# Kernel optimization log

Hardware: AMD Instinct MI355X
Metric: run time of the kernel (lower is better)

## Reference

```python
import jax, jax.numpy as jnp
import numpy as np

B, N, D, E = 8, 512, 256, 16384  # batch, num_nodes, hidden_dim, num_edges


def setup_inputs() -> dict:
    key = jax.random.key(0)
    kf, ke, k1, k2, k3, k4 = jax.random.split(key, 6)
    features = jax.random.normal(kf, (B, N, D), dtype=jnp.float32)
    edge_index = jax.random.randint(ke, (2, E), 0, N, dtype=jnp.int64)
    # weight_net: Linear(2D -> D), ReLU, Linear(D -> 1), Sigmoid
    s1 = 1.0 / np.sqrt(2 * D)
    s2 = 1.0 / np.sqrt(D)
    W1 = jax.random.uniform(k1, (2 * D, D), jnp.float32, -s1, s1)
    b1 = jax.random.uniform(k2, (D,), jnp.float32, -s1, s1)
    W2 = jax.random.uniform(k3, (D, 1), jnp.float32, -s2, s2)
    b2 = jax.random.uniform(k4, (1,), jnp.float32, -s2, s2)
    return {"features": features, "W1": W1, "b1": b1, "W2": W2, "b2": b2,
            "edge_index": edge_index}


def reference(features, W1, b1, W2, b2, edge_index):
    src, dst = edge_index[0], edge_index[1]            # [E], [E]
    fi = features[:, src]                              # [B, E, D]
    fj = features[:, dst]                              # [B, E, D]
    pair = jnp.concatenate([fi, fj], axis=-1)          # [B, E, 2D]
    h = jax.nn.relu(jnp.einsum('bef,fh->beh', pair, W1) + b1)   # [B, E, D]
    s = jax.nn.sigmoid(jnp.einsum('beh,ho->beo', h, W2) + b2)[..., 0]  # [B, E]
    bsz, n = features.shape[0], features.shape[1]
    weights = jnp.zeros((bsz, n, n), features.dtype).at[:, src, dst].set(s)
    return weights
```

## Files before the change

kernel.cpp:

```cpp
#include <hip/hip_runtime.h>
#include <hip/hip_bf16.h>
#include <cstdint>

#define B_ 8
#define N_ 512
#define D_ 256
#define E_ 16384
#define H_ 256

#define SA_STRIDE 56
#define SB_STRIDE 56
#define NSB 8
#define SUBCAP 32

using bf16x8 = __attribute__((ext_vector_type(8))) short;
using f32x4  = __attribute__((ext_vector_type(4))) float;

__device__ inline unsigned short f2bf(float f) {
    union { float f; unsigned u; } v; v.f = f;
    unsigned u = v.u;
    return (unsigned short)((u + 0x7fffu + ((u >> 16) & 1u)) >> 16);
}

__global__ __launch_bounds__(256)
void prep_k(const float* __restrict__ W1, const int* __restrict__ eidx,
            unsigned short* __restrict__ W1T,
            int* __restrict__ gCnt, int* __restrict__ gBucket) {
    const int tb = blockIdx.x, t = threadIdx.x;

    if (tb >= 32) {
        __shared__ int hist[512];
        const int sb = tb - 32;
        for (int i = t; i < 512; i += 256) hist[i] = 0;
        __syncthreads();
#pragma unroll
        for (int k = 0; k < 8; k++) {
            int e = sb * 2048 + k * 256 + t;
            int s = eidx[e];
            int d = eidx[E_ + e];
            int slot = atomicAdd(&hist[s], 1);
            gBucket[(s * NSB + sb) * SUBCAP + slot] = d;
        }
        __syncthreads();
        for (int s = t; s < 512; s += 256)
            gCnt[s * NSB + sb] = hist[s];
        return;
    }

    __shared__ float tile[64][65];
    const int h   = tb >> 4;
    const int rem = tb & 15;
    const int tk  = (rem >> 2) * 64;
    const int tn  = (rem & 3) * 64;
    const float* Wh = W1 + (size_t)h * 256 * 256;
    const int c = t & 63, r0 = t >> 6;
#pragma unroll
    for (int i = 0; i < 16; i++) {
        int r = r0 + i * 4;
        tile[r][c] = Wh[(size_t)(tk + r) * 256 + tn + c];
    }
    __syncthreads();
#pragma unroll
    for (int i = 0; i < 16; i++) {
        int rn = r0 + i * 4;
        W1T[(size_t)(h * 256 + tn + rn) * 256 + tk + c] = f2bf(tile[c][rn]);
    }
}

__global__ __launch_bounds__(256)
void node_gemm(const float* __restrict__ feat,
               const unsigned short* __restrict__ W1T,
               const float* __restrict__ b1,
               unsigned short* __restrict__ P,
               float4* __restrict__ out4) {
    __shared__ unsigned short sA[64 * SA_STRIDE];
    __shared__ unsigned short sB[256 * SB_STRIDE];

    const int t  = threadIdx.x;
    const int bm = blockIdx.x >> 1;
    const int bn = blockIdx.x & 1;
    const int m0 = bm * 64;

    {
        float4 z = make_float4(0.f, 0.f, 0.f, 0.f);
        float4* oz = out4 + (size_t)blockIdx.x * 4096 + t;
#pragma unroll
        for (int i = 0; i < 16; i++) oz[i * 256] = z;
    }

    const int arow = t >> 2;
    const int akg  = (t & 3) * 8;
    const float* pA = feat + (size_t)(m0 + arow) * 256;
    const unsigned short* pB = W1T + (size_t)(bn * 256 + t) * 256;

    const int wave = t >> 6, lane = t & 63, l15 = lane & 15, quad = lane >> 4;

    f32x4 acc[4][4];
#pragma unroll
    for (int rm = 0; rm < 4; rm++)
#pragma unroll
        for (int cn = 0; cn < 4; cn++)
            acc[rm][cn] = (f32x4){0.f, 0.f, 0.f, 0.f};

    for (int k0 = 0; k0 < 256; k0 += 32) {
        __syncthreads();
        {
            float4 lo = *(const float4*)(pA + k0 + akg);
            float4 hi = *(const float4*)(pA + k0 + akg + 4);
            union { bf16x8 v; unsigned short s[8]; } u;
            u.s[0] = f2bf(lo.x); u.s[1] = f2bf(lo.y); u.s[2] = f2bf(lo.z); u.s[3] = f2bf(lo.w);
            u.s[4] = f2bf(hi.x); u.s[5] = f2bf(hi.y); u.s[6] = f2bf(hi.z); u.s[7] = f2bf(hi.w);
            *(bf16x8*)(sA + arow * SA_STRIDE + akg) = u.v;
        }
        {
            const unsigned short* p = pB + k0;
            uint4 q0 = *(const uint4*)(p);
            uint4 q1 = *(const uint4*)(p + 8);
            uint4 q2 = *(const uint4*)(p + 16);
            uint4 q3 = *(const uint4*)(p + 24);
            *(uint4*)(sB + t * SB_STRIDE +  0) = q0;
            *(uint4*)(sB + t * SB_STRIDE +  8) = q1;
            *(uint4*)(sB + t * SB_STRIDE + 16) = q2;
            *(uint4*)(sB + t * SB_STRIDE + 24) = q3;
        }
        __syncthreads();

        bf16x8 af[4], bfr[4];
#pragma unroll
        for (int rm = 0; rm < 4; rm++)
            af[rm] = *(const bf16x8*)(sA + (rm * 16 + l15) * SA_STRIDE + quad * 8);
#pragma unroll
        for (int cn = 0; cn < 4; cn++)
            bfr[cn] = *(const bf16x8*)(sB + (wave * 64 + cn * 16 + l15) * SB_STRIDE + quad * 8);
#pragma unroll
        for (int rm = 0; rm < 4; rm++)
#pragma unroll
            for (int cn = 0; cn < 4; cn++)
                acc[rm][cn] = __builtin_amdgcn_mfma_f32_16x16x32_bf16(af[rm], bfr[cn], acc[rm][cn], 0, 0, 0);
    }

#pragma unroll
    for (int cn = 0; cn < 4; cn++) {
        int colh = wave * 64 + cn * 16 + l15;
        float bias = (bn == 0) ? b1[colh] : 0.f;
        int col = bn * 256 + colh;
#pragma unroll
        for (int rm = 0; rm < 4; rm++)
#pragma unroll
            for (int r = 0; r < 4; r++) {
                int row = m0 + rm * 16 + quad * 4 + r;
                P[(size_t)row * 512 + col] = f2bf(acc[rm][cn][r] + bias);
            }
    }
}

__device__ inline float dot8nb(uint4 qu, uint4 qv, const float* w2p) {
    unsigned us[4] = {qu.x, qu.y, qu.z, qu.w};
    unsigned vs[4] = {qv.x, qv.y, qv.z, qv.w};
    float p = 0.f;
#pragma unroll
    for (int j = 0; j < 4; j++) {
        float ulo = __uint_as_float(us[j] << 16);
        float uhi = __uint_as_float(us[j] & 0xffff0000u);
        float vlo = __uint_as_float(vs[j] << 16);
        float vhi = __uint_as_float(vs[j] & 0xffff0000u);
        float hlo = fmaxf(ulo + vlo, 0.f);
        float hhi = fmaxf(uhi + vhi, 0.f);
        p = fmaf(hlo, w2p[2 * j],     p);
        p = fmaf(hhi, w2p[2 * j + 1], p);
    }
    return p;
}

__global__ __launch_bounds__(256)
void edge_score(const unsigned short* __restrict__ P,
                const float* __restrict__ W2, const float* __restrict__ b2,
                const int* __restrict__ gCnt, const int* __restrict__ gBucket,
                float* __restrict__ out) {
    const int b     = blockIdx.x & 7;
    const int chunk = blockIdx.x >> 3;
    const int lane  = threadIdx.x & 63;
    const int wave  = threadIdx.x >> 6;
    const int g     = lane >> 4;
    const int w     = lane & 15;
    const int wid   = wave * 4 + g;
    const int s     = 2 * chunk + (wid >> 3);
    const int o     = wid & 7;

    const int* cp = gCnt + s * NSB;
    int4 c0 = *(const int4*)cp;
    int4 c1 = *(const int4*)(cp + 4);
    int pre[9];
    pre[0] = 0;
    pre[1] = pre[0] + c0.x; pre[2] = pre[1] + c0.y;
    pre[3] = pre[2] + c0.z; pre[4] = pre[3] + c0.w;
    pre[5] = pre[4] + c1.x; pre[6] = pre[5] + c1.y;
    pre[7] = pre[6] + c1.z; pre[8] = pre[7] + c1.w;
    const int en = pre[8];
    const int* bucket = gBucket + s * (NSB * SUBCAP);

    float w2r[16];
#pragma unroll
    for (int j = 0; j < 4; j++)
        *(float4*)(w2r + 4 * j) = *(const float4*)(W2 + w * 16 + 4 * j);
    const float b2v = b2[0];

    const unsigned short* Pu = P + ((size_t)b * 512 + s) * 512 + w * 16;
    uint4 u0 = *(const uint4*)(Pu);
    uint4 u1 = *(const uint4*)(Pu + 8);
    const unsigned short* Pv = P + (size_t)b * 512 * 512 + 256 + w * 16;
    float* outb = out + ((size_t)b * 512 + s) * 512;

    auto fetch = [&](int j) -> int {
        int i = 0;
#pragma unroll
        for (int q = 1; q < 8; q++) i += (j >= pre[q]);
        return bucket[i * SUBCAP + (j - pre[i])];
    };

    int j = o;
    int dst0 = 0; uint4 v00 = {}, v01 = {};
    if (j < en) {
        dst0 = fetch(j);
        const unsigned short* pv = Pv + (size_t)dst0 * 512;
        v00 = *(const uint4*)pv; v01 = *(const uint4*)(pv + 8);
    }
    while (j < en) {
        int jn = j + 8;
        int dst1 = 0; uint4 v10 = {}, v11 = {};
        if (jn < en) {
            dst1 = fetch(jn);
            const unsigned short* pv = Pv + (size_t)dst1 * 512;
            v10 = *(const uint4*)pv; v11 = *(const uint4*)(pv + 8);
        }
        float p = dot8nb(u0, v00, w2r) + dot8nb(u1, v01, w2r + 8);
        p += __shfl_xor(p, 1);
        p += __shfl_xor(p, 2);
        p += __shfl_xor(p, 4);
        p += __shfl_xor(p, 8);
        if (w == 0) {
            float sv = 1.0f / (1.0f + __expf(-(p + b2v)));
            outb[dst0] = sv;
        }
        dst0 = dst1; v00 = v10; v01 = v11; j = jn;
    }
}

extern "C" void kernel_launch(void* const* d_in, const int* in_sizes, int n_in,
                              void* d_out, int out_size, void* d_ws, size_t ws_size,
                              hipStream_t stream) {
    const float* feat = (const float*)d_in[0];
    const float* W1   = (const float*)d_in[1];
    const float* b1   = (const float*)d_in[2];
    const float* W2   = (const float*)d_in[3];
    const float* b2   = (const float*)d_in[4];
    const int*   eidx = (const int*)d_in[5];
    float* out = (float*)d_out;

    unsigned short* W1T = (unsigned short*)d_ws;
    unsigned short* P   = (unsigned short*)((char*)d_ws + (1 << 20));
    int* gCnt    = (int*)((char*)d_ws + (6 << 20));
    int* gBucket = (int*)((char*)d_ws + (6 << 20) + (1 << 16));

    prep_k<<<40, 256, 0, stream>>>(W1, eidx, W1T, gCnt, gBucket);
    node_gemm<<<128, 256, 0, stream>>>(feat, W1T, b1, P, (float4*)out);
    edge_score<<<2048, 256, 0, stream>>>(P, W2, b2, gCnt, gBucket, out);
}
```

Measured before the change: 96.82 us.

## Fuse node GEMM, bucketing and edge scoring into one persistent kernel with grid barrier

Merges the edge bucketing, node projection GEMM and edge scoring kernels into one 1024-block kernel that synchronises through a two-level atomic grid barrier, leaving a small init kernel for the W1 transpose and barrier reset. The GEMM tile shrinks to 32 rows so 256 blocks do the GEMM, and edge scoring is regrouped to 4 sources per block. The goal is to remove kernel launch gaps and the tail between stages. In exchange it risks deadlock if the 1024 blocks are not all co-resident (the code relies on launch_bounds occupancy of 4), and barrier spinning adds cost.

```diff
diff --git a/kernel.cpp b/kernel.cpp
--- a/kernel.cpp
+++ b/kernel.cpp
@@ -14,6 +14,7 @@
 #define SUBCAP 32
 
 using bf16x8 = __attribute__((ext_vector_type(8))) short;
+using bf16x4 = __attribute__((ext_vector_type(4))) short;
 using f32x4  = __attribute__((ext_vector_type(4))) float;
 
 __device__ inline unsigned short f2bf(float f) {
@@ -23,30 +24,14 @@
 }
 
 __global__ __launch_bounds__(256)
-void prep_k(const float* __restrict__ W1, const int* __restrict__ eidx,
-            unsigned short* __restrict__ W1T,
-            int* __restrict__ gCnt, int* __restrict__ gBucket) {
+void init_k(const float* __restrict__ W1, unsigned short* __restrict__ W1T,
+            int* __restrict__ bar) {
     const int tb = blockIdx.x, t = threadIdx.x;
-
-    if (tb >= 32) {
-        __shared__ int hist[512];
-        const int sb = tb - 32;
-        for (int i = t; i < 512; i += 256) hist[i] = 0;
-        __syncthreads();
-#pragma unroll
-        for (int k = 0; k < 8; k++) {
-            int e = sb * 2048 + k * 256 + t;
-            int s = eidx[e];
-            int d = eidx[E_ + e];
-            int slot = atomicAdd(&hist[s], 1);
-            gBucket[(s * NSB + sb) * SUBCAP + slot] = d;
-        }
-        __syncthreads();
-        for (int s = t; s < 512; s += 256)
-            gCnt[s * NSB + sb] = hist[s];
+    if (tb == 32) {
+#pragma unroll
+        for (int i = 0; i < 5; i++) bar[t + i * 256] = 0;
         return;
     }
-
     __shared__ float tile[64][65];
     const int h   = tb >> 4;
     const int rem = tb & 15;
@@ -67,91 +52,25 @@
     }
 }
 
-__global__ __launch_bounds__(256)
-void node_gemm(const float* __restrict__ feat,
-               const unsigned short* __restrict__ W1T,
-               const float* __restrict__ b1,
-               unsigned short* __restrict__ P,
-               float4* __restrict__ out4) {
-    __shared__ unsigned short sA[64 * SA_STRIDE];
-    __shared__ unsigned short sB[256 * SB_STRIDE];
-
-    const int t  = threadIdx.x;
-    const int bm = blockIdx.x >> 1;
-    const int bn = blockIdx.x & 1;
-    const int m0 = bm * 64;
-
-    {
-        float4 z = make_float4(0.f, 0.f, 0.f, 0.f);
-        float4* oz = out4 + (size_t)blockIdx.x * 4096 + t;
-#pragma unroll
-        for (int i = 0; i < 16; i++) oz[i * 256] = z;
-    }
-
-    const int arow = t >> 2;
-    const int akg  = (t & 3) * 8;
-    const float* pA = feat + (size_t)(m0 + arow) * 256;
-    const unsigned short* pB = W1T + (size_t)(bn * 256 + t) * 256;
-
-    const int wave = t >> 6, lane = t & 63, l15 = lane & 15, quad = lane >> 4;
-
-    f32x4 acc[4][4];
-#pragma unroll
-    for (int rm = 0; rm < 4; rm++)
-#pragma unroll
-        for (int cn = 0; cn < 4; cn++)
-            acc[rm][cn] = (f32x4){0.f, 0.f, 0.f, 0.f};
-
-    for (int k0 = 0; k0 < 256; k0 += 32) {
-        __syncthreads();
-        {
-            float4 lo = *(const float4*)(pA + k0 + akg);
-            float4 hi = *(const float4*)(pA + k0 + akg + 4);
-            union { bf16x8 v; unsigned short s[8]; } u;
-            u.s[0] = f2bf(lo.x); u.s[1] = f2bf(lo.y); u.s[2] = f2bf(lo.z); u.s[3] = f2bf(lo.w);
-            u.s[4] = f2bf(hi.x); u.s[5] = f2bf(hi.y); u.s[6] = f2bf(hi.z); u.s[7] = f2bf(hi.w);
-            *(bf16x8*)(sA + arow * SA_STRIDE + akg) = u.v;
-        }
-        {
-            const unsigned short* p = pB + k0;
-            uint4 q0 = *(const uint4*)(p);
-            uint4 q1 = *(const uint4*)(p + 8);
-            uint4 q2 = *(const uint4*)(p + 16);
-            uint4 q3 = *(const uint4*)(p + 24);
-            *(uint4*)(sB + t * SB_STRIDE +  0) = q0;
-            *(uint4*)(sB + t * SB_STRIDE +  8) = q1;
-            *(uint4*)(sB + t * SB_STRIDE + 16) = q2;
-            *(uint4*)(sB + t * SB_STRIDE + 24) = q3;
-        }
-        __syncthreads();
-
-        bf16x8 af[4], bfr[4];
-#pragma unroll
-        for (int rm = 0; rm < 4; rm++)
-            af[rm] = *(const bf16x8*)(sA + (rm * 16 + l15) * SA_STRIDE + quad * 8);
-#pragma unroll
-        for (int cn = 0; cn < 4; cn++)
-            bfr[cn] = *(const bf16x8*)(sB + (wave * 64 + cn * 16 + l15) * SB_STRIDE + quad * 8);
-#pragma unroll
-        for (int rm = 0; rm < 4; rm++)
-#pragma unroll
-            for (int cn = 0; cn < 4; cn++)
-                acc[rm][cn] = __builtin_amdgcn_mfma_f32_16x16x32_bf16(af[rm], bfr[cn], acc[rm][cn], 0, 0, 0);
-    }
-
-#pragma unroll
-    for (int cn = 0; cn < 4; cn++) {
-        int colh = wave * 64 + cn * 16 + l15;
-        float bias = (bn == 0) ? b1[colh] : 0.f;
-        int col = bn * 256 + colh;
-#pragma unroll
-        for (int rm = 0; rm < 4; rm++)
-#pragma unroll
-            for (int r = 0; r < 4; r++) {
-                int row = m0 + rm * 16 + quad * 4 + r;
-                P[(size_t)row * 512 + col] = f2bf(acc[rm][cn][r] + bias);
-            }
-    }
+__device__ inline void grid_barrier(int* bar, int bid) {
+    __syncthreads();
+    __threadfence();
+    if (threadIdx.x == 0) {
+        const int leaf = bid & 31;
+        int prev = atomicAdd(&bar[leaf * 16], 1);
+        if (prev == 31) {
+            int r = atomicAdd(&bar[512], 1);
+            if (r == 31) {
+                __threadfence();
+                for (int l = 0; l < 32; l++)
+                    atomicExch(&bar[544 + l * 16], 1);
+            }
+        }
+        while (atomicAdd(&bar[544 + leaf * 16], 0) == 0)
+            __builtin_amdgcn_s_sleep(8);
+    }
+    __syncthreads();
+    __threadfence();
 }
 
 __device__ inline float dot8nb(uint4 qu, uint4 qv, const float* w2p) {
@@ -172,77 +91,186 @@
     return p;
 }
 
-__global__ __launch_bounds__(256)
-void edge_score(const unsigned short* __restrict__ P,
-                const float* __restrict__ W2, const float* __restrict__ b2,
-                const int* __restrict__ gCnt, const int* __restrict__ gBucket,
-                float* __restrict__ out) {
-    const int b     = blockIdx.x & 7;
-    const int chunk = blockIdx.x >> 3;
-    const int lane  = threadIdx.x & 63;
-    const int wave  = threadIdx.x >> 6;
-    const int g     = lane >> 4;
-    const int w     = lane & 15;
-    const int wid   = wave * 4 + g;
-    const int s     = 2 * chunk + (wid >> 3);
-    const int o     = wid & 7;
-
-    const int* cp = gCnt + s * NSB;
-    int4 c0 = *(const int4*)cp;
-    int4 c1 = *(const int4*)(cp + 4);
-    int pre[9];
-    pre[0] = 0;
-    pre[1] = pre[0] + c0.x; pre[2] = pre[1] + c0.y;
-    pre[3] = pre[2] + c0.z; pre[4] = pre[3] + c0.w;
-    pre[5] = pre[4] + c1.x; pre[6] = pre[5] + c1.y;
-    pre[7] = pre[6] + c1.z; pre[8] = pre[7] + c1.w;
-    const int en = pre[8];
-    const int* bucket = gBucket + s * (NSB * SUBCAP);
-
-    float w2r[16];
-#pragma unroll
-    for (int j = 0; j < 4; j++)
-        *(float4*)(w2r + 4 * j) = *(const float4*)(W2 + w * 16 + 4 * j);
-    const float b2v = b2[0];
-
-    const unsigned short* Pu = P + ((size_t)b * 512 + s) * 512 + w * 16;
-    uint4 u0 = *(const uint4*)(Pu);
-    uint4 u1 = *(const uint4*)(Pu + 8);
-    const unsigned short* Pv = P + (size_t)b * 512 * 512 + 256 + w * 16;
-    float* outb = out + ((size_t)b * 512 + s) * 512;
-
-    auto fetch = [&](int j) -> int {
-        int i = 0;
-#pragma unroll
-        for (int q = 1; q < 8; q++) i += (j >= pre[q]);
-        return bucket[i * SUBCAP + (j - pre[i])];
-    };
-
-    int j = o;
-    int dst0 = 0; uint4 v00 = {}, v01 = {};
-    if (j < en) {
-        dst0 = fetch(j);
-        const unsigned short* pv = Pv + (size_t)dst0 * 512;
-        v00 = *(const uint4*)pv; v01 = *(const uint4*)(pv + 8);
-    }
-    while (j < en) {
-        int jn = j + 8;
-        int dst1 = 0; uint4 v10 = {}, v11 = {};
-        if (jn < en) {
-            dst1 = fetch(jn);
-            const unsigned short* pv = Pv + (size_t)dst1 * 512;
-            v10 = *(const uint4*)pv; v11 = *(const uint4*)(pv + 8);
-        }
-        float p = dot8nb(u0, v00, w2r) + dot8nb(u1, v01, w2r + 8);
-        p += __shfl_xor(p, 1);
-        p += __shfl_xor(p, 2);
-        p += __shfl_xor(p, 4);
-        p += __shfl_xor(p, 8);
-        if (w == 0) {
-            float sv = 1.0f / (1.0f + __expf(-(p + b2v)));
-            outb[dst0] = sv;
-        }
-        dst0 = dst1; v00 = v10; v01 = v11; j = jn;
+union SMem {
+    struct {
+        unsigned short sA[32 * SA_STRIDE];
+        unsigned short sB[256 * SB_STRIDE];
+    } g;
+    int hist[512];
+};
+
+__global__ __launch_bounds__(256, 4)
+void mega(const float* __restrict__ feat, const unsigned short* __restrict__ W1T,
+          const float* __restrict__ b1, const float* __restrict__ W2,
+          const float* __restrict__ b2, const int* __restrict__ eidx,
+          float* __restrict__ out, unsigned short* __restrict__ P,
+          int* __restrict__ gCnt8, int* __restrict__ gBucket,
+          int* __restrict__ bar) {
+    __shared__ SMem sm;
+    const int bid = blockIdx.x;
+    const int t   = threadIdx.x;
+
+    {
+        float4 z = make_float4(0.f, 0.f, 0.f, 0.f);
+        float4* oz = (float4*)out + (size_t)bid * 512 + t;
+        oz[0] = z; oz[256] = z;
+    }
+
+    if (bid >= 256 && bid < 264) {
+        const int sb = bid - 256;
+        for (int i = t; i < 512; i += 256) sm.hist[i] = 0;
+        __syncthreads();
+#pragma unroll
+        for (int k = 0; k < 8; k++) {
+            int e = sb * 2048 + k * 256 + t;
+            int s = eidx[e];
+            int d = eidx[E_ + e];
+            int slot = atomicAdd(&sm.hist[s], 1);
+            gBucket[(s * NSB + sb) * SUBCAP + slot] = d;
+        }
+        __syncthreads();
+        for (int s = t; s < 512; s += 256)
+            gCnt8[s * NSB + sb] = sm.hist[s];
+    } else if (bid < 256) {
+        const int bm = bid >> 1;
+        const int bn = bid & 1;
+        const int m0 = bm * 32;
+
+        const int arow = t >> 3;
+        const int akg  = (t & 7) * 4;
+        const float* pA = feat + (size_t)(m0 + arow) * 256;
+        const unsigned short* pB = W1T + (size_t)(bn * 256 + t) * 256;
+
+        const int wave = t >> 6, lane = t & 63, l15 = lane & 15, quad = lane >> 4;
+
+        f32x4 acc[2][4];
+#pragma unroll
+        for (int rm = 0; rm < 2; rm++)
+#pragma unroll
+            for (int cn = 0; cn < 4; cn++)
+                acc[rm][cn] = (f32x4){0.f, 0.f, 0.f, 0.f};
+
+        for (int k0 = 0; k0 < 256; k0 += 32) {
+            __syncthreads();
+            {
+                float4 lo = *(const float4*)(pA + k0 + akg);
+                union { bf16x4 v; unsigned short s[4]; } u;
+                u.s[0] = f2bf(lo.x); u.s[1] = f2bf(lo.y);
+                u.s[2] = f2bf(lo.z); u.s[3] = f2bf(lo.w);
+                *(bf16x4*)(sm.g.sA + arow * SA_STRIDE + akg) = u.v;
+            }
+            {
+                const unsigned short* p = pB + k0;
+                uint4 q0 = *(const uint4*)(p);
+                uint4 q1 = *(const uint4*)(p + 8);
+                uint4 q2 = *(const uint4*)(p + 16);
+                uint4 q3 = *(const uint4*)(p + 24);
+                *(uint4*)(sm.g.sB + t * SB_STRIDE +  0) = q0;
+                *(uint4*)(sm.g.sB + t * SB_STRIDE +  8) = q1;
+                *(uint4*)(sm.g.sB + t * SB_STRIDE + 16) = q2;
+                *(uint4*)(sm.g.sB + t * SB_STRIDE + 24) = q3;
+            }
+            __syncthreads();
+
+            bf16x8 af[2], bfr[4];
+#pragma unroll
+            for (int rm = 0; rm < 2; rm++)
+                af[rm] = *(const bf16x8*)(sm.g.sA + (rm * 16 + l15) * SA_STRIDE + quad * 8);
+#pragma unroll
+            for (int cn = 0; cn < 4; cn++)
+                bfr[cn] = *(const bf16x8*)(sm.g.sB + (wave * 64 + cn * 16 + l15) * SB_STRIDE + quad * 8);
+#pragma unroll
+            for (int rm = 0; rm < 2; rm++)
+#pragma unroll
+                for (int cn = 0; cn < 4; cn++)
+                    acc[rm][cn] = __builtin_amdgcn_mfma_f32_16x16x32_bf16(af[rm], bfr[cn], acc[rm][cn], 0, 0, 0);
+        }
+
+#pragma unroll
+        for (int cn = 0; cn < 4; cn++) {
+            int colh = wave * 64 + cn * 16 + l15;
+            float bias = (bn == 0) ? b1[colh] : 0.f;
+            int col = bn * 256 + colh;
+#pragma unroll
+            for (int rm = 0; rm < 2; rm++)
+#pragma unroll
+                for (int r = 0; r < 4; r++) {
+                    int row = m0 + rm * 16 + quad * 4 + r;
+                    P[(size_t)row * 512 + col] = f2bf(acc[rm][cn][r] + bias);
+                }
+        }
+    }
+
+    grid_barrier(bar, bid);
+
+    {
+        const int b    = bid & 7;
+        const int q    = bid >> 3;
+        const int lane = t & 63;
+        const int wave = t >> 6;
+        const int g    = lane >> 4;
+        const int w    = lane & 15;
+        const int wid  = wave * 4 + g;
+        const int s    = q * 4 + (wid >> 2);
+        const int o    = wid & 3;
+
+        const int* cp = gCnt8 + s * NSB;
+        int4 c0 = *(const int4*)cp;
+        int4 c1 = *(const int4*)(cp + 4);
+        int pre[9];
+        pre[0] = 0;
+        pre[1] = pre[0] + c0.x; pre[2] = pre[1] + c0.y;
+        pre[3] = pre[2] + c0.z; pre[4] = pre[3] + c0.w;
+        pre[5] = pre[4] + c1.x; pre[6] = pre[5] + c1.y;
+        pre[7] = pre[6] + c1.z; pre[8] = pre[7] + c1.w;
+        const int en = pre[8];
+        const int* bucket = gBucket + s * (NSB * SUBCAP);
+
+        float w2r[16];
+#pragma unroll
+        for (int j = 0; j < 4; j++)
+            *(float4*)(w2r + 4 * j) = *(const float4*)(W2 + w * 16 + 4 * j);
+        const float b2v = b2[0];
+
+        const unsigned short* Pu = P + ((size_t)b * 512 + s) * 512 + w * 16;
+        uint4 u0 = *(const uint4*)(Pu);
+        uint4 u1 = *(const uint4*)(Pu + 8);
+        const unsigned short* Pv = P + (size_t)b * 512 * 512 + 256 + w * 16;
+        float* outb = out + ((size_t)b * 512 + s) * 512;
+
+        auto fetch = [&](int j) -> int {
+            int i = 0;
+#pragma unroll
+            for (int qq = 1; qq < 8; qq++) i += (j >= pre[qq]);
+            return bucket[i * SUBCAP + (j - pre[i])];
+        };
+
+        int j = o;
+        int dst0 = 0; uint4 v00 = {}, v01 = {};
+        if (j < en) {
+            dst0 = fetch(j);
+            const unsigned short* pv = Pv + (size_t)dst0 * 512;
+            v00 = *(const uint4*)pv; v01 = *(const uint4*)(pv + 8);
+        }
+        while (j < en) {
+            int jn = j + 4;
+            int dst1 = 0; uint4 v10 = {}, v11 = {};
+            if (jn < en) {
+                dst1 = fetch(jn);
+                const unsigned short* pv = Pv + (size_t)dst1 * 512;
+                v10 = *(const uint4*)pv; v11 = *(const uint4*)(pv + 8);
+            }
+            float p = dot8nb(u0, v00, w2r) + dot8nb(u1, v01, w2r + 8);
+            p += __shfl_xor(p, 1);
+            p += __shfl_xor(p, 2);
+            p += __shfl_xor(p, 4);
+            p += __shfl_xor(p, 8);
+            if (w == 0) {
+                float sv = 1.0f / (1.0f + __expf(-(p + b2v)));
+                outb[dst0] = sv;
+            }
+            dst0 = dst1; v00 = v10; v01 = v11; j = jn;
+        }
     }
 }
 
@@ -259,10 +287,11 @@
 
     unsigned short* W1T = (unsigned short*)d_ws;
     unsigned short* P   = (unsigned short*)((char*)d_ws + (1 << 20));
-    int* gCnt    = (int*)((char*)d_ws + (6 << 20));
+    int* gCnt8   = (int*)((char*)d_ws + (6 << 20));
     int* gBucket = (int*)((char*)d_ws + (6 << 20) + (1 << 16));
-
-    prep_k<<<40, 256, 0, stream>>>(W1, eidx, W1T, gCnt, gBucket);
-    node_gemm<<<128, 256, 0, stream>>>(feat, W1T, b1, P, (float4*)out);
-    edge_score<<<2048, 256, 0, stream>>>(P, W2, b2, gCnt, gBucket, out);
-}
+    int* bar     = (int*)((char*)d_ws + (7 << 20));
+
+    init_k<<<33, 256, 0, stream>>>(W1, W1T, bar);
+    mega<<<1024, 256, 0, stream>>>(feat, W1T, b1, W2, b2, eidx,
+                                   out, P, gCnt8, gBucket, bar);
+}
```

Result: slower. 242.2 us (+150.2%).
